# Performance work log

Hardware: AMD Instinct MI355X
Metric: run time of the kernel (lower is better)

## Reference

```python
import jax, jax.numpy as jnp
import numpy as np

N_EMBD = 1024
N_HEAD = 16

def setup_inputs() -> dict:
    key = jax.random.key(0)
    k1, k2, k3 = jax.random.split(key, 3)
    x = jax.random.normal(k1, (2, 2048, N_EMBD), dtype=jnp.float32)
    # torch Linear(n, 3n): y = x @ W_attn (we store transposed weight directly)
    w_attn = jax.random.normal(k2, (N_EMBD, 3 * N_EMBD), dtype=jnp.float32) * 0.02
    w_proj = jax.random.normal(k3, (N_EMBD, N_EMBD), dtype=jnp.float32) * 0.02
    return {"x": x, "w_attn": w_attn, "w_proj": w_proj}

def reference(x, w_attn, w_proj):
    B, S, E = x.shape
    H = N_HEAD
    D = E // H
    qkv = x @ w_attn  # [B, S, 3E]
    q, k, v = jnp.split(qkv, 3, axis=-1)
    # [B, H, S, D]
    q = q.reshape(B, S, H, D).transpose(0, 2, 1, 3)
    k = k.reshape(B, S, H, D).transpose(0, 2, 1, 3)
    v = v.reshape(B, S, H, D).transpose(0, 2, 1, 3)
    scale = 1.0 / jnp.sqrt(jnp.asarray(D, dtype=x.dtype))
    a = jnp.einsum('bhqd,bhkd->bhqk', q, k) * scale  # [B, H, S, S]
    causal = jnp.tril(jnp.ones((S, S), dtype=bool))
    a = jnp.where(causal, a, -jnp.inf)
    a = jax.nn.softmax(a, axis=-1)
    y = jnp.einsum('bhqk,bhkd->bhqd', a, v)  # [B, H, S, D]
    y = y.transpose(0, 2, 1, 3).reshape(B, S, E)
    return y @ w_proj
```

## Files before the change

### kernel.cpp

```cpp
#include <hip/hip_runtime.h>

#define DEVI __device__ __forceinline__

typedef short bf16x8 __attribute__((ext_vector_type(8)));
typedef float f32x4 __attribute__((ext_vector_type(4)));
typedef unsigned short u16;
typedef unsigned int u32;

static constexpr int Bn = 2, S = 2048, E = 1024, H = 16, D = 64;
static constexpr int Mrows = Bn * S;
static constexpr int N_QKV = 3 * E;

DEVI u16 f2b(float f) {
  union { float f; u32 u; } c; c.f = f;
  return (u16)((c.u + 0x7FFFu + ((c.u >> 16) & 1u)) >> 16);
}

DEVI bf16x8 ld8(const u16* p) {
  union { uint4 u; bf16x8 v; } c;
  c.u = *reinterpret_cast<const uint4*>(p);
  return c.v;
}

#define MFMA(a, b, c) __builtin_amdgcn_mfma_f32_16x16x32_bf16(a, b, c, 0, 0, 0)

#define G2L16(gptr, lptr) \
  __builtin_amdgcn_global_load_lds((const __attribute__((address_space(1))) void*)(gptr), \
                                   (__attribute__((address_space(3))) void*)(lptr), 16, 0, 0)

__global__ __launch_bounds__(256) void prep(const float* __restrict__ x,
                                            const float* __restrict__ w_attn,
                                            const float* __restrict__ w_proj,
                                            u16* __restrict__ xb, u16* __restrict__ wabT,
                                            u16* __restrict__ wpbT) {
  __shared__ float t[32][33];
  int blk = blockIdx.x, tid = threadIdx.x;
  if (blk >= 4096) {
    int i = (blk - 4096) * 256 + tid;
    float4 f = reinterpret_cast<const float4*>(x)[i];
    ushort4 u;
    u.x = f2b(f.x); u.y = f2b(f.y); u.z = f2b(f.z); u.w = f2b(f.w);
    reinterpret_cast<ushort4*>(xb)[i] = u;
    return;
  }
  const float* in; u16* out; int R, C, bx, by;
  if (blk < 3072) {
    in = w_attn; out = wabT; R = E; C = N_QKV;
    bx = (blk % 96) * 32; by = (blk / 96) * 32;
  } else {
    int q = blk - 3072;
    in = w_proj; out = wpbT; R = E; C = E;
    bx = (q % 32) * 32; by = (q / 32) * 32;
  }
  int tx = tid & 31, ty = tid >> 5;
#pragma unroll
  for (int k = 0; k < 32; k += 8)
    t[ty + k][tx] = in[(size_t)(by + ty + k) * C + bx + tx];
  __syncthreads();
#pragma unroll
  for (int k = 0; k < 32; k += 8)
    out[(size_t)(bx + ty + k) * R + by + tx] = f2b(t[tx][ty + k]);
}

__global__ __launch_bounds__(256) void gemm_qkv(const u16* __restrict__ A, const u16* __restrict__ BT,
                                                u16* __restrict__ Qb, u16* __restrict__ Kb,
                                                u16* __restrict__ VbT) {
  constexpr int K = 1024, BK = 64;
  __shared__ __align__(16) u16 As[128 * BK];
  __shared__ __align__(16) u16 Bs[64 * BK];
  int tid = threadIdx.x;
  int w = tid >> 6, lane = tid & 63, quad = lane >> 4, l15 = lane & 15;
  int m0 = blockIdx.x * 128, n0 = blockIdx.y * 64;
  int mw = (w >> 1) * 64, nw = (w & 1) * 32;
  const u16* Ab = A + (size_t)m0 * K;
  const u16* Bb = BT + (size_t)n0 * K;
  f32x4 acc[4][2] = {};
  for (int k0 = 0; k0 < K; k0 += BK) {
#pragma unroll
    for (int j = 0; j < 4; j++) {
      int L = j * 256 + tid;
      int row = L >> 3, cg = (L & 7) ^ (row & 7);
      G2L16(Ab + (size_t)row * K + k0 + cg * 8, (char*)As + L * 16);
    }
#pragma unroll
    for (int j = 0; j < 2; j++) {
      int L = j * 256 + tid;
      int row = L >> 3, cg = (L & 7) ^ (row & 7);
      G2L16(Bb + (size_t)row * K + k0 + cg * 8, (char*)Bs + L * 16);
    }
    __syncthreads();
#pragma unroll
    for (int kk = 0; kk < 2; kk++) {
      int sg = ((kk << 2) | quad) ^ (l15 & 7);
      bf16x8 a[4], b[2];
#pragma unroll
      for (int i = 0; i < 4; i++) a[i] = ld8(&As[(mw + i * 16 + l15) * BK + sg * 8]);
#pragma unroll
      for (int i = 0; i < 2; i++) b[i] = ld8(&Bs[(nw + i * 16 + l15) * BK + sg * 8]);
#pragma unroll
      for (int mb = 0; mb < 4; mb++)
#pragma unroll
        for (int nb = 0; nb < 2; nb++)
          acc[mb][nb] = MFMA(a[mb], b[nb], acc[mb][nb]);
    }
    __syncthreads();
  }
#pragma unroll
  for (int mb = 0; mb < 4; mb++) {
    int m = m0 + mw + mb * 16 + quad * 4;
    int b = m >> 11, s = m & 2047;
#pragma unroll
    for (int nb = 0; nb < 2; nb++) {
      int n = n0 + nw + nb * 16 + l15;
      int sec = n >> 10, e = n & 1023, h = e >> 6, d = e & 63;
      int bh = b * H + h;
      if (sec == 0) {
#pragma unroll
        for (int r = 0; r < 4; r++)
          Qb[((size_t)bh * S + s + r) * D + d] = f2b(acc[mb][nb][r] * 0.1803368801111244f);
      } else if (sec == 1) {
#pragma unroll
        for (int r = 0; r < 4; r++)
          Kb[((size_t)bh * S + s + r) * D + d] = f2b(acc[mb][nb][r]);
      } else {
        ushort4 v;
        v.x = f2b(acc[mb][nb][0]); v.y = f2b(acc[mb][nb][1]);
        v.z = f2b(acc[mb][nb][2]); v.w = f2b(acc[mb][nb][3]);
        *reinterpret_cast<ushort4*>(VbT + ((size_t)bh * D + d) * S + s) = v;
      }
    }
  }
}

__global__ __launch_bounds__(256, 3) void attn(const u16* __restrict__ Qb, const u16* __restrict__ Kb,
                                               const u16* __restrict__ VbT, u16* __restrict__ Yb) {
  __shared__ __align__(16) u16 Ks[128 * 64];
  __shared__ __align__(16) u16 Vs[64 * 128];
  __shared__ __align__(16) u32 Ps[4][16 * 68];
  int w = threadIdx.x >> 6, lane = threadIdx.x & 63, quad = lane >> 4, l15 = lane & 15;
  int bh = blockIdx.x & 31, qt = 31 - (blockIdx.x >> 5);
  int b = bh >> 4, h = bh & 15;
  int nc = (qt + 2) >> 1;

  const u16* Kbh = Kb + (size_t)bh * S * D;
  const u16* Vbh = VbT + (size_t)bh * D * S;
  u32* myP = &Ps[w][0];
  const u16* myP16 = (const u16*)myP;
  int prow = l15 * 68 + quad * 2;

  int q_base = qt * 64 + w * 16;
  int qrow = q_base + l15;
  int kmax = q_base + 16;

  const u16* Qp = Qb + ((size_t)bh * S + qrow) * D + quad * 8;
  bf16x8 bq0 = ld8(Qp), bq1 = ld8(Qp + 32);

  float lpart = 0.f;
  f32x4 o[4] = {};

  for (int c = 0; c < nc; c++) {
    int kbase = c * 128;
    __syncthreads();
    const u16* Kg = Kbh + (size_t)kbase * D;
#pragma unroll
    for (int j = 0; j < 4; j++) {
      int L = (w * 4 + j) * 64 + lane;
      int row = L >> 3, cg = (L & 7) ^ (row & 7);
      G2L16(Kg + (size_t)row * 64 + cg * 8, (char*)Ks + L * 16);
    }
    const u16* Vg = Vbh + kbase;
#pragma unroll
    for (int j = 0; j < 4; j++) {
      int L = (w * 4 + j) * 64 + lane;
      int row = L >> 4, cg = (L & 15) ^ (row & 15);
      G2L16(Vg + (size_t)row * S + cg * 8, (char*)Vs + L * 16);
    }
    __syncthreads();

#pragma unroll
    for (int mb = 0; mb < 8; mb++) {
      int kb = kbase + mb * 16;
      u32 pa = 0, pb = 0;
      if (kb < kmax) {
        int row = mb * 16 + l15;
        bf16x8 ak0 = ld8(&Ks[row * 64 + ((quad ^ (row & 7)) * 8)]);
        bf16x8 ak1 = ld8(&Ks[row * 64 + (((quad + 4) ^ (row & 7)) * 8)]);
        f32x4 z = {};
        z = MFMA(ak0, bq0, z);
        z = MFMA(ak1, bq1, z);
        if (kb == q_base) {
#pragma unroll
          for (int r = 0; r < 4; r++)
            if (quad * 4 + r > l15) z[r] = -1e30f;
        }
        float p0 = __builtin_amdgcn_exp2f(z[0]);
        float p1 = __builtin_amdgcn_exp2f(z[1]);
        float p2 = __builtin_amdgcn_exp2f(z[2]);
        float p3 = __builtin_amdgcn_exp2f(z[3]);
        lpart += (p0 + p1) + (p2 + p3);
        union { float f; u32 u; } c0, c1, c2, c3;
        c0.f = p0; c1.f = p1; c2.f = p2; c3.f = p3;
        pa = __builtin_amdgcn_perm(c1.u + 0x8000u, c0.u + 0x8000u, 0x07060302u);
        pb = __builtin_amdgcn_perm(c3.u + 0x8000u, c2.u + 0x8000u, 0x07060302u);
      }
      uint2 pw; pw.x = pa; pw.y = pb;
      *reinterpret_cast<uint2*>(&myP[prow + mb * 8]) = pw;
    }
#pragma unroll
    for (int ch = 0; ch < 4; ch++) {
      if (kbase + ch * 32 < kmax) {
        bf16x8 bp = ld8(myP16 + l15 * 136 + ch * 32 + quad * 8);
#pragma unroll
        for (int dd = 0; dd < 4; dd++) {
          int rv = dd * 16 + l15;
          bf16x8 av = ld8(&Vs[rv * 128 + (((ch * 4 + quad) ^ (rv & 15)) * 8)]);
          o[dd] = MFMA(av, bp, o[dd]);
        }
      }
    }
  }

  float l = lpart;
  l += __shfl_xor(l, 16);
  l += __shfl_xor(l, 32);
  float rinv = 1.0f / l;
  u16* Yp = Yb + ((size_t)b * S + qrow) * E + h * 64 + quad * 4;
#pragma unroll
  for (int dd = 0; dd < 4; dd++) {
    ushort4 y;
    y.x = f2b(o[dd][0] * rinv); y.y = f2b(o[dd][1] * rinv);
    y.z = f2b(o[dd][2] * rinv); y.w = f2b(o[dd][3] * rinv);
    *reinterpret_cast<ushort4*>(Yp + dd * 16) = y;
  }
}

__global__ __launch_bounds__(256) void gemm_proj(const u16* __restrict__ A, const u16* __restrict__ BT,
                                                 float* __restrict__ out) {
  constexpr int K = 1024, BK = 64;
  __shared__ __align__(16) u16 As[128 * BK];
  __shared__ __align__(16) u16 Bs[64 * BK];
  int tid = threadIdx.x;
  int w = tid >> 6, lane = tid & 63, quad = lane >> 4, l15 = lane & 15;
  int m0 = blockIdx.x * 128, n0 = blockIdx.y * 64;
  int mw = (w >> 1) * 64, nw = (w & 1) * 32;
  const u16* Ab = A + (size_t)m0 * K;
  const u16* Bb = BT + (size_t)n0 * K;
  f32x4 acc[4][2] = {};
  for (int k0 = 0; k0 < K; k0 += BK) {
#pragma unroll
    for (int j = 0; j < 4; j++) {
      int L = j * 256 + tid;
      int row = L >> 3, cg = (L & 7) ^ (row & 7);
      G2L16(Ab + (size_t)row * K + k0 + cg * 8, (char*)As + L * 16);
    }
#pragma unroll
    for (int j = 0; j < 2; j++) {
      int L = j * 256 + tid;
      int row = L >> 3, cg = (L & 7) ^ (row & 7);
      G2L16(Bb + (size_t)row * K + k0 + cg * 8, (char*)Bs + L * 16);
    }
    __syncthreads();
#pragma unroll
    for (int kk = 0; kk < 2; kk++) {
      int sg = ((kk << 2) | quad) ^ (l15 & 7);
      bf16x8 a[4], b[2];
#pragma unroll
      for (int i = 0; i < 4; i++) a[i] = ld8(&As[(mw + i * 16 + l15) * BK + sg * 8]);
#pragma unroll
      for (int i = 0; i < 2; i++) b[i] = ld8(&Bs[(nw + i * 16 + l15) * BK + sg * 8]);
#pragma unroll
      for (int mb = 0; mb < 4; mb++)
#pragma unroll
        for (int nb = 0; nb < 2; nb++)
          acc[mb][nb] = MFMA(a[mb], b[nb], acc[mb][nb]);
    }
    __syncthreads();
  }
#pragma unroll
  for (int mb = 0; mb < 4; mb++) {
    int m = m0 + mw + mb * 16 + quad * 4;
#pragma unroll
    for (int nb = 0; nb < 2; nb++) {
      int n = n0 + nw + nb * 16 + l15;
#pragma unroll
      for (int r = 0; r < 4; r++)
        out[(size_t)(m + r) * E + n] = acc[mb][nb][r];
    }
  }
}

extern "C" void kernel_launch(void* const* d_in, const int* in_sizes, int n_in,
                              void* d_out, int out_size, void* d_ws, size_t ws_size,
                              hipStream_t stream) {
  const float* x = (const float*)d_in[0];
  const float* w_attn = (const float*)d_in[1];
  const float* w_proj = (const float*)d_in[2];
  float* out = (float*)d_out;
  char* ws = (char*)d_ws;

  u16* xb   = (u16*)(ws);
  u16* wabT = (u16*)(ws + 8388608);
  u16* wpbT = (u16*)(ws + 14680064);
  u16* Qb   = (u16*)(ws + 16777216);
  u16* Kb   = (u16*)(ws + 25165824);
  u16* VbT  = (u16*)(ws + 33554432);
  u16* Yb   = (u16*)(ws + 41943040);

  prep<<<8192, 256, 0, stream>>>(x, w_attn, w_proj, xb, wabT, wpbT);
  gemm_qkv<<<dim3(Mrows / 128, N_QKV / 64), 256, 0, stream>>>(xb, wabT, Qb, Kb, VbT);
  attn<<<Bn * H * (S / 64), 256, 0, stream>>>(Qb, Kb, VbT, Yb);
  gemm_proj<<<dim3(Mrows / 128, E / 64), 256, 0, stream>>>(Yb, wpbT, out);
}
```

Measured before the change: 165.9 us.

## Load K/V directly from global per wave with 32-row Q tiles per wave

The attention kernel drops the shared-memory K/V staging and block-wide barriers. Each wave now handles two 16-row query tiles and reads K and V fragments straight from global/L2, reusing each fragment across both tiles. It also raises the occupancy hint, halves the grid, and adds MFMA priority hints. The aim is to remove barrier stalls and LDS traffic, at the cost of redundant global loads across waves and likely unbalanced causal work within a block.

```diff
diff --git a/kernel.cpp b/kernel.cpp
--- a/kernel.cpp
+++ b/kernel.cpp
@@ -132,63 +132,49 @@
   }
 }
 
-__global__ __launch_bounds__(256, 3) void attn(const u16* __restrict__ Qb, const u16* __restrict__ Kb,
+__global__ __launch_bounds__(256, 4) void attn(const u16* __restrict__ Qb, const u16* __restrict__ Kb,
                                                const u16* __restrict__ VbT, u16* __restrict__ Yb) {
-  __shared__ __align__(16) u16 Ks[128 * 64];
-  __shared__ __align__(16) u16 Vs[64 * 128];
-  __shared__ __align__(16) u32 Ps[4][16 * 68];
+  __shared__ __align__(16) u32 Ps[4][2][16 * 68];
   int w = threadIdx.x >> 6, lane = threadIdx.x & 63, quad = lane >> 4, l15 = lane & 15;
-  int bh = blockIdx.x & 31, qt = 31 - (blockIdx.x >> 5);
+  int bh = blockIdx.x & 31, qt = 15 - (blockIdx.x >> 5);
   int b = bh >> 4, h = bh & 15;
-  int nc = (qt + 2) >> 1;
 
   const u16* Kbh = Kb + (size_t)bh * S * D;
   const u16* Vbh = VbT + (size_t)bh * D * S;
-  u32* myP = &Ps[w][0];
-  const u16* myP16 = (const u16*)myP;
+  u32* myP0 = &Ps[w][0][0];
+  u32* myP1 = &Ps[w][1][0];
+  const u16* myP16 = (const u16*)myP0;
   int prow = l15 * 68 + quad * 2;
 
-  int q_base = qt * 64 + w * 16;
-  int qrow = q_base + l15;
-  int kmax = q_base + 16;
-
-  const u16* Qp = Qb + ((size_t)bh * S + qrow) * D + quad * 8;
-  bf16x8 bq0 = ld8(Qp), bq1 = ld8(Qp + 32);
-
-  float lpart = 0.f;
-  f32x4 o[4] = {};
-
+  int qw = qt * 128 + w * 32;
+  int qrow0 = qw + l15;
+
+  const u16* Qp = Qb + ((size_t)bh * S + qrow0) * D + quad * 8;
+  bf16x8 q00 = ld8(Qp), q01 = ld8(Qp + 32);
+  bf16x8 q10 = ld8(Qp + (size_t)16 * D), q11 = ld8(Qp + (size_t)16 * D + 32);
+
+  float lp0 = 0.f, lp1 = 0.f;
+  f32x4 o0[4] = {}, o1[4] = {};
+
+  int nc = (qw + 32 + 127) >> 7;
   for (int c = 0; c < nc; c++) {
     int kbase = c * 128;
-    __syncthreads();
-    const u16* Kg = Kbh + (size_t)kbase * D;
-#pragma unroll
-    for (int j = 0; j < 4; j++) {
-      int L = (w * 4 + j) * 64 + lane;
-      int row = L >> 3, cg = (L & 7) ^ (row & 7);
-      G2L16(Kg + (size_t)row * 64 + cg * 8, (char*)Ks + L * 16);
-    }
-    const u16* Vg = Vbh + kbase;
-#pragma unroll
-    for (int j = 0; j < 4; j++) {
-      int L = (w * 4 + j) * 64 + lane;
-      int row = L >> 4, cg = (L & 15) ^ (row & 15);
-      G2L16(Vg + (size_t)row * S + cg * 8, (char*)Vs + L * 16);
-    }
-    __syncthreads();
-
 #pragma unroll
     for (int mb = 0; mb < 8; mb++) {
       int kb = kbase + mb * 16;
+      bf16x8 ak0, ak1;
+      if (kb <= qw + 16) {
+        const u16* Kg = Kbh + (size_t)(kb + l15) * D + quad * 8;
+        ak0 = ld8(Kg); ak1 = ld8(Kg + 32);
+      }
       u32 pa = 0, pb = 0;
-      if (kb < kmax) {
-        int row = mb * 16 + l15;
-        bf16x8 ak0 = ld8(&Ks[row * 64 + ((quad ^ (row & 7)) * 8)]);
-        bf16x8 ak1 = ld8(&Ks[row * 64 + (((quad + 4) ^ (row & 7)) * 8)]);
+      if (kb <= qw) {
         f32x4 z = {};
-        z = MFMA(ak0, bq0, z);
-        z = MFMA(ak1, bq1, z);
-        if (kb == q_base) {
+        __builtin_amdgcn_s_setprio(1);
+        z = MFMA(ak0, q00, z);
+        z = MFMA(ak1, q01, z);
+        __builtin_amdgcn_s_setprio(0);
+        if (kb == qw) {
 #pragma unroll
           for (int r = 0; r < 4; r++)
             if (quad * 4 + r > l15) z[r] = -1e30f;
@@ -197,40 +183,73 @@
         float p1 = __builtin_amdgcn_exp2f(z[1]);
         float p2 = __builtin_amdgcn_exp2f(z[2]);
         float p3 = __builtin_amdgcn_exp2f(z[3]);
-        lpart += (p0 + p1) + (p2 + p3);
+        lp0 += (p0 + p1) + (p2 + p3);
         union { float f; u32 u; } c0, c1, c2, c3;
         c0.f = p0; c1.f = p1; c2.f = p2; c3.f = p3;
         pa = __builtin_amdgcn_perm(c1.u + 0x8000u, c0.u + 0x8000u, 0x07060302u);
         pb = __builtin_amdgcn_perm(c3.u + 0x8000u, c2.u + 0x8000u, 0x07060302u);
       }
-      uint2 pw; pw.x = pa; pw.y = pb;
-      *reinterpret_cast<uint2*>(&myP[prow + mb * 8]) = pw;
+      { uint2 pw; pw.x = pa; pw.y = pb;
+        *reinterpret_cast<uint2*>(&myP0[prow + mb * 8]) = pw; }
+      pa = 0; pb = 0;
+      if (kb <= qw + 16) {
+        f32x4 z = {};
+        __builtin_amdgcn_s_setprio(1);
+        z = MFMA(ak0, q10, z);
+        z = MFMA(ak1, q11, z);
+        __builtin_amdgcn_s_setprio(0);
+        if (kb == qw + 16) {
+#pragma unroll
+          for (int r = 0; r < 4; r++)
+            if (quad * 4 + r > l15) z[r] = -1e30f;
+        }
+        float p0 = __builtin_amdgcn_exp2f(z[0]);
+        float p1 = __builtin_amdgcn_exp2f(z[1]);
+        float p2 = __builtin_amdgcn_exp2f(z[2]);
+        float p3 = __builtin_amdgcn_exp2f(z[3]);
+        lp1 += (p0 + p1) + (p2 + p3);
+        union { float f; u32 u; } c0, c1, c2, c3;
+        c0.f = p0; c1.f = p1; c2.f = p2; c3.f = p3;
+        pa = __builtin_amdgcn_perm(c1.u + 0x8000u, c0.u + 0x8000u, 0x07060302u);
+        pb = __builtin_amdgcn_perm(c3.u + 0x8000u, c2.u + 0x8000u, 0x07060302u);
+      }
+      { uint2 pw; pw.x = pa; pw.y = pb;
+        *reinterpret_cast<uint2*>(&myP1[prow + mb * 8]) = pw; }
     }
 #pragma unroll
     for (int ch = 0; ch < 4; ch++) {
-      if (kbase + ch * 32 < kmax) {
-        bf16x8 bp = ld8(myP16 + l15 * 136 + ch * 32 + quad * 8);
+      int kc = kbase + ch * 32;
+      if (kc < qw + 32) {
+        bool do0 = kc < qw + 16;
+        bf16x8 bp1 = ld8(myP16 + 2176 + l15 * 136 + ch * 32 + quad * 8);
+        bf16x8 bp0;
+        if (do0) bp0 = ld8(myP16 + l15 * 136 + ch * 32 + quad * 8);
+        __builtin_amdgcn_s_setprio(1);
 #pragma unroll
         for (int dd = 0; dd < 4; dd++) {
-          int rv = dd * 16 + l15;
-          bf16x8 av = ld8(&Vs[rv * 128 + (((ch * 4 + quad) ^ (rv & 15)) * 8)]);
-          o[dd] = MFMA(av, bp, o[dd]);
+          bf16x8 av = ld8(Vbh + (size_t)(dd * 16 + l15) * S + kc + quad * 8);
+          o1[dd] = MFMA(av, bp1, o1[dd]);
+          if (do0) o0[dd] = MFMA(av, bp0, o0[dd]);
         }
-      }
-    }
-  }
-
-  float l = lpart;
-  l += __shfl_xor(l, 16);
-  l += __shfl_xor(l, 32);
-  float rinv = 1.0f / l;
-  u16* Yp = Yb + ((size_t)b * S + qrow) * E + h * 64 + quad * 4;
+        __builtin_amdgcn_s_setprio(0);
+      }
+    }
+  }
+
+  lp0 += __shfl_xor(lp0, 16); lp0 += __shfl_xor(lp0, 32);
+  lp1 += __shfl_xor(lp1, 16); lp1 += __shfl_xor(lp1, 32);
+  float r0 = 1.0f / lp0, r1 = 1.0f / lp1;
+  u16* Yp0 = Yb + ((size_t)b * S + qrow0) * E + h * 64 + quad * 4;
+  u16* Yp1 = Yp0 + (size_t)16 * E;
 #pragma unroll
   for (int dd = 0; dd < 4; dd++) {
     ushort4 y;
-    y.x = f2b(o[dd][0] * rinv); y.y = f2b(o[dd][1] * rinv);
-    y.z = f2b(o[dd][2] * rinv); y.w = f2b(o[dd][3] * rinv);
-    *reinterpret_cast<ushort4*>(Yp + dd * 16) = y;
+    y.x = f2b(o0[dd][0] * r0); y.y = f2b(o0[dd][1] * r0);
+    y.z = f2b(o0[dd][2] * r0); y.w = f2b(o0[dd][3] * r0);
+    *reinterpret_cast<ushort4*>(Yp0 + dd * 16) = y;
+    y.x = f2b(o1[dd][0] * r1); y.y = f2b(o1[dd][1] * r1);
+    y.z = f2b(o1[dd][2] * r1); y.w = f2b(o1[dd][3] * r1);
+    *reinterpret_cast<ushort4*>(Yp1 + dd * 16) = y;
   }
 }
 
@@ -308,6 +327,6 @@
 
   prep<<<8192, 256, 0, stream>>>(x, w_attn, w_proj, xb, wabT, wpbT);
   gemm_qkv<<<dim3(Mrows / 128, N_QKV / 64), 256, 0, stream>>>(xb, wabT, Qb, Kb, VbT);
-  attn<<<Bn * H * (S / 64), 256, 0, stream>>>(Qb, Kb, VbT, Yb);
+  attn<<<Bn * H * (S / 128), 256, 0, stream>>>(Qb, Kb, VbT, Yb);
   gemm_proj<<<dim3(Mrows / 128, E / 64), 256, 0, stream>>>(Yb, wpbT, out);
 }
```

Measured after the change: 356.4 us. +114.8%, slower.

## Double-buffer K/V tiles in attention with 64-key chunks and async prefetch

Applied to the files above, without the earlier changes.

Splits the attention kernel's K/V staging into 64-key chunks held in two LDS buffers. The next chunk's global-to-LDS copy is issued before computing on the current one, using explicit vmcnt waits and raw barriers in place of two __syncthreads per chunk. It also raises wave priority around the MFMA sequences. The goal is to overlap K/V loads with compute and avoid causal over-fetch. The cost is twice as many loop iterations and barriers, and the code relies on the vmcnt(4) count matching the number of outstanding G2L16 ops.

```diff
diff --git a/kernel.cpp b/kernel.cpp
--- a/kernel.cpp
+++ b/kernel.cpp
@@ -134,19 +134,18 @@
 
 __global__ __launch_bounds__(256, 3) void attn(const u16* __restrict__ Qb, const u16* __restrict__ Kb,
                                                const u16* __restrict__ VbT, u16* __restrict__ Yb) {
-  __shared__ __align__(16) u16 Ks[128 * 64];
-  __shared__ __align__(16) u16 Vs[64 * 128];
-  __shared__ __align__(16) u32 Ps[4][16 * 68];
+  __shared__ __align__(16) u16 Ks[2][64 * 64];
+  __shared__ __align__(16) u16 Vs[2][64 * 64];
+  __shared__ __align__(16) u32 Ps[4][16 * 36];
   int w = threadIdx.x >> 6, lane = threadIdx.x & 63, quad = lane >> 4, l15 = lane & 15;
   int bh = blockIdx.x & 31, qt = 31 - (blockIdx.x >> 5);
   int b = bh >> 4, h = bh & 15;
-  int nc = (qt + 2) >> 1;
+  int nc = qt + 1;
 
   const u16* Kbh = Kb + (size_t)bh * S * D;
   const u16* Vbh = VbT + (size_t)bh * D * S;
   u32* myP = &Ps[w][0];
   const u16* myP16 = (const u16*)myP;
-  int prow = l15 * 68 + quad * 2;
 
   int q_base = qt * 64 + w * 16;
   int qrow = q_base + l15;
@@ -158,36 +157,60 @@
   float lpart = 0.f;
   f32x4 o[4] = {};
 
+#pragma unroll
+  for (int j = 0; j < 2; j++) {
+    int L = (w * 2 + j) * 64 + lane;
+    int row = L >> 3, cg = (L & 7) ^ (row & 7);
+    G2L16(Kbh + (size_t)row * D + cg * 8, (char*)Ks[0] + L * 16);
+  }
+#pragma unroll
+  for (int j = 0; j < 2; j++) {
+    int L = (w * 2 + j) * 64 + lane;
+    int row = L >> 3, cg = (L & 7) ^ (row & 7);
+    G2L16(Vbh + (size_t)row * S + cg * 8, (char*)Vs[0] + L * 16);
+  }
+
   for (int c = 0; c < nc; c++) {
-    int kbase = c * 128;
-    __syncthreads();
-    const u16* Kg = Kbh + (size_t)kbase * D;
-#pragma unroll
-    for (int j = 0; j < 4; j++) {
-      int L = (w * 4 + j) * 64 + lane;
-      int row = L >> 3, cg = (L & 7) ^ (row & 7);
-      G2L16(Kg + (size_t)row * 64 + cg * 8, (char*)Ks + L * 16);
-    }
-    const u16* Vg = Vbh + kbase;
-#pragma unroll
-    for (int j = 0; j < 4; j++) {
-      int L = (w * 4 + j) * 64 + lane;
-      int row = L >> 4, cg = (L & 15) ^ (row & 15);
-      G2L16(Vg + (size_t)row * S + cg * 8, (char*)Vs + L * 16);
-    }
-    __syncthreads();
-
-#pragma unroll
-    for (int mb = 0; mb < 8; mb++) {
+    int kbase = c * 64;
+    int cur = c & 1;
+    if (c + 1 < nc) {
+      const u16* Kg = Kbh + (size_t)(kbase + 64) * D;
+      const u16* Vg = Vbh + (kbase + 64);
+#pragma unroll
+      for (int j = 0; j < 2; j++) {
+        int L = (w * 2 + j) * 64 + lane;
+        int row = L >> 3, cg = (L & 7) ^ (row & 7);
+        G2L16(Kg + (size_t)row * D + cg * 8, (char*)Ks[cur ^ 1] + L * 16);
+      }
+#pragma unroll
+      for (int j = 0; j < 2; j++) {
+        int L = (w * 2 + j) * 64 + lane;
+        int row = L >> 3, cg = (L & 7) ^ (row & 7);
+        G2L16(Vg + (size_t)row * S + cg * 8, (char*)Vs[cur ^ 1] + L * 16);
+      }
+      asm volatile("s_waitcnt vmcnt(4)" ::: "memory");
+    } else {
+      asm volatile("s_waitcnt vmcnt(0)" ::: "memory");
+    }
+    __builtin_amdgcn_s_barrier();
+    __builtin_amdgcn_sched_barrier(0);
+
+    const u16* Kc = Ks[cur];
+    const u16* Vc = Vs[cur];
+
+#pragma unroll
+    for (int mb = 0; mb < 4; mb++) {
       int kb = kbase + mb * 16;
       u32 pa = 0, pb = 0;
       if (kb < kmax) {
         int row = mb * 16 + l15;
-        bf16x8 ak0 = ld8(&Ks[row * 64 + ((quad ^ (row & 7)) * 8)]);
-        bf16x8 ak1 = ld8(&Ks[row * 64 + (((quad + 4) ^ (row & 7)) * 8)]);
+        bf16x8 ak0 = ld8(&Kc[row * 64 + ((quad ^ (row & 7)) * 8)]);
+        bf16x8 ak1 = ld8(&Kc[row * 64 + (((quad + 4) ^ (row & 7)) * 8)]);
         f32x4 z = {};
+        __builtin_amdgcn_s_setprio(1);
         z = MFMA(ak0, bq0, z);
         z = MFMA(ak1, bq1, z);
+        __builtin_amdgcn_s_setprio(0);
         if (kb == q_base) {
 #pragma unroll
           for (int r = 0; r < 4; r++)
@@ -204,20 +227,25 @@
         pb = __builtin_amdgcn_perm(c3.u + 0x8000u, c2.u + 0x8000u, 0x07060302u);
       }
       uint2 pw; pw.x = pa; pw.y = pb;
-      *reinterpret_cast<uint2*>(&myP[prow + mb * 8]) = pw;
-    }
-#pragma unroll
-    for (int ch = 0; ch < 4; ch++) {
-      if (kbase + ch * 32 < kmax) {
-        bf16x8 bp = ld8(myP16 + l15 * 136 + ch * 32 + quad * 8);
+      *reinterpret_cast<uint2*>(&myP[l15 * 36 + quad * 2 + mb * 8]) = pw;
+    }
+#pragma unroll
+    for (int ch = 0; ch < 2; ch++) {
+      int kc = kbase + ch * 32;
+      if (kc < kmax) {
+        bf16x8 bp = ld8(myP16 + l15 * 72 + ch * 32 + quad * 8);
+        __builtin_amdgcn_s_setprio(1);
 #pragma unroll
         for (int dd = 0; dd < 4; dd++) {
           int rv = dd * 16 + l15;
-          bf16x8 av = ld8(&Vs[rv * 128 + (((ch * 4 + quad) ^ (rv & 15)) * 8)]);
+          bf16x8 av = ld8(&Vc[rv * 64 + (((ch * 4 + quad) ^ (rv & 7)) * 8)]);
           o[dd] = MFMA(av, bp, o[dd]);
         }
-      }
-    }
+        __builtin_amdgcn_s_setprio(0);
+      }
+    }
+    asm volatile("s_waitcnt lgkmcnt(0)" ::: "memory");
+    __builtin_amdgcn_s_barrier();
   }
 
   float l = lpart;
```

Result: slower. 171.9 us (+3.6%).
